# Performance work log

Hardware: AMD Instinct MI355X
Metric: run time of the kernel (lower is better)

The kernel has to match this reference:

```python
import jax, jax.numpy as jnp
import numpy as np

DIM = 192
HEADS = 6
HEAD_DIM = DIM // HEADS
WS = 8            # window size
N = WS * WS       # tokens per window
IN_CC = 16        # top-k kept keys per query
B, H, W = 8, 64, 64
NEG = -100.0      # value used by the torch code for masked logits
EPS_NORM = 1e-12  # F.normalize eps
EPS_LN = 1e-5     # nn.LayerNorm eps


def _rel_pos_index(ws):
    coords = np.stack(np.meshgrid(np.arange(ws), np.arange(ws), indexing='ij'))  # (2,ws,ws)
    cf = coords.reshape(2, -1)
    rel = (cf[:, :, None] - cf[:, None, :]).transpose(1, 2, 0).astype(np.int64)  # (N,N,2)
    rel[:, :, 0] += ws - 1
    rel[:, :, 1] += ws - 1
    rel[:, :, 0] *= 2 * ws - 1
    return jnp.asarray(rel.sum(-1))  # (N,N) indices into (2ws-1)^2 table

REL_IDX = _rel_pos_index(WS)


def _layer_norm(x, g, b):
    mu = jnp.mean(x, -1, keepdims=True)
    var = jnp.mean(jnp.square(x - mu), -1, keepdims=True)
    return (x - mu) * jax.lax.rsqrt(var + EPS_LN) * g + b


def _l2n(x):
    n = jnp.sqrt(jnp.sum(jnp.square(x), -1, keepdims=True))
    return x / jnp.maximum(n, EPS_NORM)


def setup_inputs() -> dict:
    key = jax.random.key(0)
    ks = jax.random.split(key, 8)
    s = 0.02
    return {
        'x': jax.random.normal(ks[0], (B, DIM, H, W), jnp.float32),
        'norm1_g': jnp.ones((DIM,), jnp.float32),
        'norm1_b': jnp.zeros((DIM,), jnp.float32),
        'qkv_w': jax.random.normal(ks[1], (3 * DIM, DIM), jnp.float32) * s,
        'qkv_b': jnp.zeros((3 * DIM,), jnp.float32),
        'proj_w': jax.random.normal(ks[2], (DIM, DIM), jnp.float32) * s,
        'proj_b': jnp.zeros((DIM,), jnp.float32),
        'rpb_table': jax.random.normal(ks[3], ((2 * WS - 1) ** 2, HEADS), jnp.float32) * s,
        'temperature': jnp.ones((HEADS, 1, 1), jnp.float32),
        'norm2_g': jnp.ones((DIM,), jnp.float32),
        'norm2_b': jnp.zeros((DIM,), jnp.float32),
        'fc1_w': jax.random.normal(ks[4], (4 * DIM, DIM), jnp.float32) * s,
        'fc1_b': jnp.zeros((4 * DIM,), jnp.float32),
        'fc2_w': jax.random.normal(ks[5], (DIM, 4 * DIM), jnp.float32) * s,
        'fc2_b': jnp.zeros((DIM,), jnp.float32),
    }


def reference(x, norm1_g, norm1_b, qkv_w, qkv_b, proj_w, proj_b, rpb_table,
              temperature, norm2_g, norm2_b, fc1_w, fc1_b, fc2_w, fc2_b):
    b, c, h, w = x.shape
    # (B,C,H,W) -> (B,L,C), pre-norm (note: the torch code norms the shortcut too)
    xs = jnp.transpose(x.reshape(b, c, h * w), (0, 2, 1))
    shortcut = _layer_norm(xs, norm1_g, norm1_b)  # (B,L,C)

    # window partition: (B,H,W,C) -> (B*nWh*nWw, N, C); shift_size=0, no padding (H,W % WS == 0)
    xin = shortcut.reshape(b, h // WS, WS, w // WS, WS, c)
    xin = jnp.transpose(xin, (0, 1, 3, 2, 4, 5)).reshape(-1, N, c)
    B_ = xin.shape[0]

    qkv = (xin @ qkv_w.T + qkv_b).reshape(B_, N, 3, HEADS, HEAD_DIM)
    qkv = jnp.transpose(qkv, (2, 0, 3, 1, 4))  # (3, B_, h, N, d)
    q, k, v = qkv[0], qkv[1], qkv[2]

    # cosine attention with learned per-head temperature
    attn = jnp.einsum('bhnd,bhmd->bhnm', _l2n(q), _l2n(k)) * temperature  # (B_,h,N,N)

    # top-k sparsification: keep IN_CC largest logits per query (threshold == kth value;
    # equivalent to the torch topk+scatter mask for distinct values)
    kth = jax.lax.top_k(attn, IN_CC)[0][..., -1:]
    attn = jnp.where(attn >= kth, attn, NEG)

    # relative position bias gather: (N,N,h) -> (h,N,N)
    rpb = jnp.transpose(rpb_table[REL_IDX], (2, 0, 1))
    attn = jax.nn.softmax(attn + rpb[None], axis=-1)

    out = jnp.einsum('bhnm,bhmd->bhnd', attn, v)
    out = jnp.transpose(out, (0, 2, 1, 3)).reshape(B_, N, c)
    out = out @ proj_w.T + proj_b

    # window reverse -> (B, L, C)
    out = out.reshape(b, h // WS, w // WS, WS, WS, c)
    out = jnp.transpose(out, (0, 1, 3, 2, 4, 5)).reshape(b, h * w, c)

    x2 = shortcut + out  # drop_path = identity (eval)
    hdn = _layer_norm(x2, norm2_g, norm2_b)
    hdn = jax.nn.gelu(hdn @ fc1_w.T + fc1_b, approximate=False) @ fc2_w.T + fc2_b
    x2 = x2 + hdn

    # back to (B,C,H,W)
    return jnp.transpose(x2, (0, 2, 1)).reshape(b, c, h, w)
```

## Files before the change

### kernel.cpp

```cpp
#include <hip/hip_runtime.h>
#include <hip/hip_bf16.h>
#include <math.h>

#define DIM     192
#define HEADS   6
#define HEAD_DIM 32
#define NTOK    64
#define IN_CC   16
#define TTOT    32768
#define NWIN    512

using bf16x8 = __attribute__((ext_vector_type(8))) short;
using f32x4  = __attribute__((ext_vector_type(4))) float;
typedef unsigned short ushort_t;

__device__ __forceinline__ ushort_t f2bt(float f) {
    unsigned u = __float_as_uint(f);
    u += 0x7fffu + ((u >> 16) & 1u);
    return (ushort_t)(u >> 16);
}
__device__ __forceinline__ unsigned pk2t(float a, float b) {
    return (unsigned)f2bt(a) | ((unsigned)f2bt(b) << 16);
}
__device__ __forceinline__ ushort_t f2b(float f) {
    __bf16 h = (__bf16)f;
    ushort_t u;
    __builtin_memcpy(&u, &h, 2);
    return u;
}
__device__ __forceinline__ unsigned pk2(float a, float b) {
    return (unsigned)f2b(a) | ((unsigned)f2b(b) << 16);
}
__device__ __forceinline__ float b2f(ushort_t u) {
    return __uint_as_float(((unsigned)u) << 16);
}
__device__ __forceinline__ float m3(float a, float b, float c) {
    return fmaxf(fmaxf(a, b), c);
}

__global__ __launch_bounds__(256) void prep_kernel(
    const float* __restrict__ s0, const float* __restrict__ s1,
    const float* __restrict__ s2, const float* __restrict__ s3,
    ushort_t* __restrict__ d0, ushort_t* __restrict__ d1,
    ushort_t* __restrict__ d2, ushort_t* __restrict__ d3,
    const float* __restrict__ x, const float* __restrict__ g,
    const float* __restrict__ bb, ushort_t* __restrict__ outh)
{
    __shared__ float xs[64][193];
    __shared__ float mu_s[64], rs_s[64];
    __shared__ float gs[192], bs[192];
    const int bid = blockIdx.x;
    const int tid = threadIdx.x;

    if (bid < 432) {
        const float* src; ushort_t* dst; int off, K; bool perm = false;
        if (bid < 108)      { src = s0; dst = d0; off = bid;       K = 192; perm = true; }
        else if (bid < 144) { src = s1; dst = d1; off = bid - 108; K = 192; }
        else if (bid < 288) { src = s2; dst = d2; off = bid - 144; K = 192; }
        else                { src = s3; dst = d3; off = bid - 288; K = 768; }
        const int K8 = K >> 3;
        const int d  = (off * 256 + tid) * 4;
        const int frag = d >> 7, win = d & 127;
        const int m16w = win >> 3, k7 = win & 7;
        const int oblk = frag / K8, kblk = frag - oblk * K8;
        const int o = oblk * 16 + m16w, k = kblk * 8 + k7;
        int so = o;
        if (perm && o < 384) {
            const int s = o & 31;
            const int c = (((s >> 2) & 3) << 3) | (((s >> 4) & 1) << 2) | (s & 3);
            so = (o & ~31) | c;
        }
        float4 v = *(const float4*)(src + (size_t)so * K + k);
        ushort4 ov;
        ov.x = f2b(v.x); ov.y = f2b(v.y); ov.z = f2b(v.z); ov.w = f2b(v.w);
        *(ushort4*)(dst + d) = ov;
        return;
    }

    const int t0  = (bid - 432) * 64;
    const int b   = t0 >> 12;
    const int hw0 = t0 & 4095;
    if (tid < 192) { gs[tid] = g[tid]; bs[tid] = bb[tid]; }
    const int tok = tid & 63, qq = tid >> 6;
    const float* xb = x + (size_t)b * (DIM * 4096) + hw0 + tok;
    #pragma unroll
    for (int it = 0; it < 48; ++it) {
        int c = it * 4 + qq;
        xs[tok][c] = xb[(size_t)c * 4096];
    }
    __syncthreads();
    const int tok2 = tid >> 2, p = tid & 3;
    float sum = 0.f;
    #pragma unroll
    for (int c = 0; c < 48; ++c) sum += xs[tok2][p * 48 + c];
    sum += __shfl_xor(sum, 1);
    sum += __shfl_xor(sum, 2);
    const float m = sum * (1.0f / 192.0f);
    float ss = 0.f;
    #pragma unroll
    for (int c = 0; c < 48; ++c) { float d = xs[tok2][p * 48 + c] - m; ss += d * d; }
    ss += __shfl_xor(ss, 1);
    ss += __shfl_xor(ss, 2);
    if (p == 0) {
        mu_s[tok2] = m;
        rs_s[tok2] = 1.0f / sqrtf(ss * (1.0f / 192.0f) + 1e-5f);
    }
    __syncthreads();
    ushort_t* obh = outh + (size_t)t0 * DIM;
    #pragma unroll
    for (int it = 0; it < 48; ++it) {
        int idx = it * 256 + tid;
        int tk = idx / 192, c = idx % 192;
        obh[idx] = f2b((xs[tk][c] - mu_s[tk]) * rs_s[tk] * gs[c] + bs[c]);
    }
}

__global__ __launch_bounds__(768, 3) void attn_fused(
    const ushort_t* __restrict__ sc_h, const ushort_t* __restrict__ wqf,
    const float* __restrict__ qkv_b, const float* __restrict__ rpb_table,
    const float* __restrict__ temp, const ushort_t* __restrict__ wpf,
    const float* __restrict__ proj_b, float* __restrict__ x2)
{
    __shared__ __align__(16) char smem[127680];
    const int tid  = threadIdx.x;
    const int wave = tid >> 6, n = tid & 63;

    char* Rb = smem + wave * 4608;
    float*    Ssq = (float*)Rb;
    ushort_t* Ph  = (ushort_t*)Rb;
    char* Ab = smem + 55296 + wave * 5120;
    ushort_t* Vt  = (ushort_t*)Ab;
    float*    ksb = (float*)(Ab + 4608);
    float*    qnb = (float*)(Ab + 4864);
    float*    rpb = (float*)(smem + 116736) + wave * 228;

    const int wloc = (wave >= 6) ? 1 : 0;
    const int h    = wave - 6 * wloc;
    ushort_t* tile = (ushort_t*)(smem + wloc * 25600);
    ushort_t (*AoT)[200] = (ushort_t(*)[200])(smem + wloc * 25600);
    float* Cwi = (float*)(smem + 55296 + wave * 2304);

    const int win = blockIdx.x * 2 + wloc;
    const int b   = win >> 6;
    const int wh  = (win >> 3) & 7, ww = win & 7;
    const int wb  = b * 4096 + wh * 512 + ww * 8;
    const int i1  = n >> 3, j1 = n & 7;
    const int m16 = n & 15, quad = n >> 4;

    for (int r = n; r < 225; r += 64) rpb[r] = rpb_table[r * 6 + h];

    #pragma unroll
    for (int l = 0; l < 4; ++l) {
        const int g = h * 256 + l * 64 + n;
        const int t = (g * 2731) >> 16;
        const int r = g - t * 24;
        const int tt = wb + ((t >> 3) << 6) + (t & 7);
        uint4 v = *(const uint4*)(sc_h + (size_t)tt * 192 + r * 8);
        *(uint4*)(tile + t * 200 + r * 8) = v;
    }
    __syncthreads();

    const ushort_t* tb = tile + m16 * 200 + quad * 8;
    f32x4 pq[4][2], pk[4][2];
    #pragma unroll
    for (int i = 0; i < 4; ++i)
        #pragma unroll
        for (int j = 0; j < 2; ++j) { pq[i][j] = (f32x4)(0.0f); pk[i][j] = (f32x4)(0.0f); }
    {
        const ushort_t* WbQ = wqf + (size_t)(2 * h) * 3072 + m16 * 8;
        const ushort_t* WbK = wqf + (size_t)(12 + 2 * h) * 3072 + m16 * 8;
        for (int ks = 0; ks < 192; ks += 32) {
            bf16x8 af[4], wq2[2], wk2[2];
            #pragma unroll
            for (int i = 0; i < 4; ++i)
                af[i] = *(const bf16x8*)(tb + i * 3200 + ks);
            #pragma unroll
            for (int j = 0; j < 2; ++j) {
                wq2[j] = *(const bf16x8*)(WbQ + (size_t)(j * 24 + (ks >> 3) + quad) * 128);
                wk2[j] = *(const bf16x8*)(WbK + (size_t)(j * 24 + (ks >> 3) + quad) * 128);
            }
            #pragma unroll
            for (int i = 0; i < 4; ++i)
                #pragma unroll
                for (int j = 0; j < 2; ++j) {
                    pq[i][j] = __builtin_amdgcn_mfma_f32_16x16x32_bf16(wq2[j], af[i], pq[i][j], 0, 0, 0);
                    pk[i][j] = __builtin_amdgcn_mfma_f32_16x16x32_bf16(wk2[j], af[i], pk[i][j], 0, 0, 0);
                }
        }
    }
    bf16x8 qA[4], kB[4];
    #pragma unroll
    for (int part = 0; part < 2; ++part) {
        const int o0 = part * 192 + h * 32;
        const float4 bv0 = *(const float4*)&qkv_b[o0 + 8 * quad];
        const float4 bv1 = *(const float4*)&qkv_b[o0 + 8 * quad + 4];
        float ssq[4];
        #pragma unroll
        for (int i = 0; i < 4; ++i) {
            f32x4 v0 = part ? pk[i][0] : pq[i][0];
            f32x4 v1 = part ? pk[i][1] : pq[i][1];
            v0[0] += bv0.x; v0[1] += bv0.y; v0[2] += bv0.z; v0[3] += bv0.w;
            v1[0] += bv1.x; v1[1] += bv1.y; v1[2] += bv1.z; v1[3] += bv1.w;
            float sq = 0.f;
            #pragma unroll
            for (int r = 0; r < 4; ++r) sq += v0[r] * v0[r] + v1[r] * v1[r];
            ssq[i] = sq;
            bf16x8 fr;
            fr[0] = (short)f2bt(v0[0]); fr[1] = (short)f2bt(v0[1]);
            fr[2] = (short)f2bt(v0[2]); fr[3] = (short)f2bt(v0[3]);
            fr[4] = (short)f2bt(v1[0]); fr[5] = (short)f2bt(v1[1]);
            fr[6] = (short)f2bt(v1[2]); fr[7] = (short)f2bt(v1[3]);
            if (part == 0) qA[i] = fr; else kB[i] = fr;
        }
        #pragma unroll
        for (int i = 0; i < 4; ++i) {
            ssq[i] += __shfl_xor(ssq[i], 16);
            ssq[i] += __shfl_xor(ssq[i], 32);
        }
        if (quad == 0) {
            #pragma unroll
            for (int i = 0; i < 4; ++i) {
                if (part == 0) qnb[16 * i + m16] = ssq[i];
                else           ksb[4 * m16 + i]  = 1.0f / fmaxf(sqrtf(ssq[i]), 1e-12f);
            }
        }
    }

    f32x4 acc[4][4];
    #pragma unroll
    for (int i = 0; i < 4; ++i)
        #pragma unroll
        for (int j = 0; j < 4; ++j)
            acc[i][j] = __builtin_amdgcn_mfma_f32_16x16x32_bf16(qA[i], kB[j], (f32x4)(0.0f), 0, 0, 0);

    {
        f32x4 pv[4][2];
        #pragma unroll
        for (int i = 0; i < 4; ++i)
            #pragma unroll
            for (int j = 0; j < 2; ++j) pv[i][j] = (f32x4)(0.0f);
        const ushort_t* WbV = wqf + (size_t)(24 + 2 * h) * 3072 + m16 * 8;
        for (int ks = 0; ks < 192; ks += 32) {
            bf16x8 af[4], wv2[2];
            #pragma unroll
            for (int i = 0; i < 4; ++i)
                af[i] = *(const bf16x8*)(tb + i * 3200 + ks);
            #pragma unroll
            for (int j = 0; j < 2; ++j)
                wv2[j] = *(const bf16x8*)(WbV + (size_t)(j * 24 + (ks >> 3) + quad) * 128);
            #pragma unroll
            for (int i = 0; i < 4; ++i)
                #pragma unroll
                for (int j = 0; j < 2; ++j)
                    pv[i][j] = __builtin_amdgcn_mfma_f32_16x16x32_bf16(wv2[j], af[i], pv[i][j], 0, 0, 0);
        }
        const int o0 = 384 + h * 32;
        const float4 bv0 = *(const float4*)&qkv_b[o0 + quad * 4];
        const float4 bv1 = *(const float4*)&qkv_b[o0 + 16 + quad * 4];
        #pragma unroll
        for (int i = 0; i < 4; ++i) {
            f32x4 v0 = pv[i][0], v1 = pv[i][1];
            v0[0] += bv0.x; v0[1] += bv0.y; v0[2] += bv0.z; v0[3] += bv0.w;
            v1[0] += bv1.x; v1[1] += bv1.y; v1[2] += bv1.z; v1[3] += bv1.w;
            #pragma unroll
            for (int r = 0; r < 4; ++r) {
                Vt[(quad * 4 + r) * 72 + 4 * m16 + i]      = f2bt(v0[r]);
                Vt[(16 + quad * 4 + r) * 72 + 4 * m16 + i] = f2bt(v1[r]);
            }
        }
    }

    __syncthreads();

    float s[64];
    #pragma unroll
    for (int i = 0; i < 4; ++i) {
        #pragma unroll
        for (int r = 0; r < 4; ++r) {
            f32x4 vv = { acc[i][0][r], acc[i][1][r], acc[i][2][r], acc[i][3][r] };
            *(f32x4*)&Ssq[(4 * quad + r) * 68 + 4 * m16] = vv;
        }
        if ((n >> 4) == i) {
            #pragma unroll
            for (int c = 0; c < 16; ++c)
                *(float4*)&s[4 * c] = *(const float4*)&Ssq[(n & 15) * 68 + 4 * c];
        }
    }

    const float qs = temp[h] / fmaxf(sqrtf(qnb[n]), 1e-12f);
    #pragma unroll
    for (int c = 0; c < 16; ++c) {
        float4 kv = *(const float4*)&ksb[4 * c];
        s[4*c+0] *= qs * kv.x; s[4*c+1] *= qs * kv.y;
        s[4*c+2] *= qs * kv.z; s[4*c+3] *= qs * kv.w;
    }

    float thr = 1e30f;
    for (int it = 0; it < IN_CC; ++it) {
        #define MK(c) ((s[(c)] < thr) ? s[(c)] : -1e30f)
        float w[22];
        #pragma unroll
        for (int g = 0; g < 21; ++g) w[g] = m3(MK(3*g), MK(3*g+1), MK(3*g+2));
        w[21] = MK(63);
        #undef MK
        float y[8];
        #pragma unroll
        for (int g = 0; g < 7; ++g) y[g] = m3(w[3*g], w[3*g+1], w[3*g+2]);
        y[7] = w[21];
        thr = m3(m3(y[0], y[1], y[2]), m3(y[3], y[4], y[5]), fmaxf(y[6], y[7]));
    }

    const int basen = i1 * 15 + j1;
    float mxp[8];
    #pragma unroll
    for (int c = 0; c < 64; ++c) {
        const int m = 16 * (c & 3) + (c >> 2);
        const int i2 = m >> 3, j2 = m & 7;
        float vv = ((s[c] >= thr) ? s[c] : -100.0f)
                 + rpb[basen + (7 - i2) * 15 + (7 - j2)];
        s[c] = vv;
        if (c < 8) mxp[c] = vv; else mxp[c & 7] = fmaxf(mxp[c & 7], vv);
    }
    const float mx = m3(m3(mxp[0], mxp[1], mxp[2]), m3(mxp[3], mxp[4], mxp[5]),
                        fmaxf(mxp[6], mxp[7]));
    float sum = 0.f;
    #pragma unroll
    for (int c = 0; c < 64; ++c) { float e = __expf(s[c] - mx); s[c] = e; sum += e; }
    const float inv = 1.0f / sum;
    #pragma unroll
    for (int c = 0; c < 64; ++c) s[c] *= inv;

    bf16x8 vb[2][2];
    #pragma unroll
    for (int kh2 = 0; kh2 < 2; ++kh2)
        #pragma unroll
        for (int j2 = 0; j2 < 2; ++j2)
            vb[kh2][j2] = *(const bf16x8*)&Vt[(16 * j2 + m16) * 72 + kh2 * 32 + quad * 8];

    f32x4 o[4][2];
    #pragma unroll
    for (int i = 0; i < 4; ++i)
        #pragma unroll
        for (int j2 = 0; j2 < 2; ++j2)
            o[i][j2] = (f32x4)(0.0f);
    #pragma unroll
    for (int hf = 0; hf < 2; ++hf) {
        if ((n >> 5) == hf) {
            #pragma unroll
            for (int g = 0; g < 8; ++g) {
                uint4 w;
                w.x = pk2t(s[8*g+0], s[8*g+1]); w.y = pk2t(s[8*g+2], s[8*g+3]);
                w.z = pk2t(s[8*g+4], s[8*g+5]); w.w = pk2t(s[8*g+6], s[8*g+7]);
                *(uint4*)&Ph[(n & 31) * 72 + 8 * g] = w;
            }
        }
        #pragma unroll
        for (int ih = 0; ih < 2; ++ih) {
            const int i = 2 * hf + ih;
            #pragma unroll
            for (int kh2 = 0; kh2 < 2; ++kh2) {
                bf16x8 pafr = *(const bf16x8*)&Ph[(16 * ih + m16) * 72 + kh2 * 32 + quad * 8];
                o[i][0] = __builtin_amdgcn_mfma_f32_16x16x32_bf16(pafr, vb[kh2][0], o[i][0], 0, 0, 0);
                o[i][1] = __builtin_amdgcn_mfma_f32_16x16x32_bf16(pafr, vb[kh2][1], o[i][1], 0, 0, 0);
            }
        }
    }
    __syncthreads();

    #pragma unroll
    for (int i = 0; i < 4; ++i) {
        #pragma unroll
        for (int r = 0; r < 4; ++r) {
            const int row = 16 * i + 4 * quad + r;
            AoT[row][h * 32 + m16]      = f2bt(o[i][0][r]);
            AoT[row][h * 32 + 16 + m16] = f2bt(o[i][1][r]);
        }
    }
    __syncthreads();

    const int r8 = n >> 3, c4 = (n & 7) * 4;
    uint2 rv[4][2];
    #pragma unroll
    for (int i = 0; i < 4; ++i)
        #pragma unroll
        for (int q = 0; q < 2; ++q) {
            const int tok = 16 * i + 8 * q + r8;
            const int tt = wb + ((tok >> 3) << 6) + (tok & 7);
            rv[i][q] = *(const uint2*)(sc_h + (size_t)tt * 192 + h * 32 + c4);
        }

    f32x4 pacc[4][2];
    #pragma unroll
    for (int i = 0; i < 4; ++i)
        #pragma unroll
        for (int j = 0; j < 2; ++j)
            pacc[i][j] = (f32x4)(0.0f);
    const ushort_t* Wb = wpf + (size_t)(h * 2) * 24 * 128 + m16 * 8;
    for (int ks = 0; ks < 192; ks += 32) {
        bf16x8 af[4], wv[2];
        #pragma unroll
        for (int i = 0; i < 4; ++i)
            af[i] = *(const bf16x8*)&AoT[16 * i + m16][quad * 8 + ks];
        #pragma unroll
        for (int j = 0; j < 2; ++j)
            wv[j] = *(const bf16x8*)(Wb + (size_t)(j * 24 + (ks >> 3) + quad) * 128);
        #pragma unroll
        for (int i = 0; i < 4; ++i)
            #pragma unroll
            for (int j = 0; j < 2; ++j)
                pacc[i][j] = __builtin_amdgcn_mfma_f32_16x16x32_bf16(wv[j], af[i], pacc[i][j], 0, 0, 0);
    }

    const float4 bj0 = *(const float4*)&proj_b[h * 32 + quad * 4];
    const float4 bj1 = *(const float4*)&proj_b[h * 32 + 16 + quad * 4];
    #pragma unroll
    for (int i = 0; i < 4; ++i) {
        f32x4 v0 = pacc[i][0], v1 = pacc[i][1];
        v0[0] += bj0.x; v0[1] += bj0.y; v0[2] += bj0.z; v0[3] += bj0.w;
        v1[0] += bj1.x; v1[1] += bj1.y; v1[2] += bj1.z; v1[3] += bj1.w;
        *(f32x4*)&Cwi[m16 * 36 + quad * 4]      = v0;
        *(f32x4*)&Cwi[m16 * 36 + 16 + quad * 4] = v1;
        #pragma unroll
        for (int q = 0; q < 2; ++q) {
            const int row = 8 * q + r8;
            const int tok = 16 * i + row;
            const int tt = wb + ((tok >> 3) << 6) + (tok & 7);
            float4 vv = *(const float4*)&Cwi[row * 36 + c4];
            const uint2 rr = rv[i][q];
            vv.x += b2f((ushort_t)(rr.x & 0xffffu));
            vv.y += b2f((ushort_t)(rr.x >> 16));
            vv.z += b2f((ushort_t)(rr.y & 0xffffu));
            vv.w += b2f((ushort_t)(rr.y >> 16));
            *(float4*)&x2[(size_t)tt * DIM + h * 32 + c4] = vv;
        }
    }
}

__global__ __launch_bounds__(768, 3) void mlp_fused(
    const float* __restrict__ x2, const ushort_t* __restrict__ w1f,
    const ushort_t* __restrict__ w2f, const float* __restrict__ fc1_b,
    const float* __restrict__ fc2_b, const float* __restrict__ g2,
    const float* __restrict__ b2, float* __restrict__ outp)
{
    __shared__ __align__(16) char smem[103936];
    ushort_t (*h_h)[200] = (ushort_t(*)[200])smem;
    ushort_t (*a1c)[200] = (ushort_t(*)[200])(smem + 51200);
    float* gs = (float*)(smem + 102400);
    float* bs = gs + 192;

    const int tid  = threadIdx.x;
    const int wave = tid >> 6, lane = tid & 63;
    const int m16 = lane & 15, quad = lane >> 4;
    const int half = wave / 6, ow = wave - 6 * half;
    const int t0  = blockIdx.x * 128;
    const int b   = t0 >> 12;
    const int hw0 = t0 & 4095;

    if (tid < 192) { gs[tid] = g2[tid]; bs[tid] = b2[tid]; }
    __syncthreads();
    if (tid < 512) {
        const int tok = tid >> 2, p = tid & 3;
        const float* rp = x2 + (size_t)(t0 + tok) * DIM + p * 48;
        float xv[48];
        #pragma unroll
        for (int c4 = 0; c4 < 12; ++c4)
            *(float4*)&xv[c4 * 4] = *(const float4*)(rp + c4 * 4);
        float sum = 0.f;
        #pragma unroll
        for (int c = 0; c < 48; ++c) sum += xv[c];
        sum += __shfl_xor(sum, 1);
        sum += __shfl_xor(sum, 2);
        const float m = sum * (1.0f / 192.0f);
        float ss = 0.f;
        #pragma unroll
        for (int c = 0; c < 48; ++c) { float d = xv[c] - m; ss += d * d; }
        ss += __shfl_xor(ss, 1);
        ss += __shfl_xor(ss, 2);
        const float rs = 1.0f / sqrtf(ss * (1.0f / 192.0f) + 1e-5f);
        ushort_t* hp = &h_h[tok][p * 48];
        #pragma unroll
        for (int c2 = 0; c2 < 24; ++c2) {
            float v0 = (xv[2*c2]   - m) * rs * gs[p * 48 + 2*c2]   + bs[p * 48 + 2*c2];
            float v1 = (xv[2*c2+1] - m) * rs * gs[p * 48 + 2*c2+1] + bs[p * 48 + 2*c2+1];
            *(unsigned*)(hp + 2 * c2) = pk2(v0, v1);
        }
    }
    __syncthreads();

    f32x4 acc2[4][2];
    #pragma unroll
    for (int i = 0; i < 4; ++i)
        #pragma unroll
        for (int j = 0; j < 2; ++j)
            acc2[i][j] = (f32x4)(0.0f);

    for (int c = 0; c < 4; ++c) {
        f32x4 acc1[4][2];
        #pragma unroll
        for (int i = 0; i < 4; ++i)
            #pragma unroll
            for (int j = 0; j < 2; ++j)
                acc1[i][j] = (f32x4)(0.0f);
        const ushort_t* Wb1 = w1f + (size_t)(c * 12 + ow * 2) * 3072 + m16 * 8;
        for (int ks = 0; ks < 192; ks += 32) {
            bf16x8 af[4], wv[2];
            #pragma unroll
            for (int i = 0; i < 4; ++i)
                af[i] = *(const bf16x8*)&h_h[half * 64 + 16 * i + m16][quad * 8 + ks];
            #pragma unroll
            for (int j = 0; j < 2; ++j)
                wv[j] = *(const bf16x8*)(Wb1 + (size_t)(j * 24 + (ks >> 3) + quad) * 128);
            #pragma unroll
            for (int i = 0; i < 4; ++i)
                #pragma unroll
                for (int j = 0; j < 2; ++j)
                    acc1[i][j] = __builtin_amdgcn_mfma_f32_16x16x32_bf16(wv[j], af[i], acc1[i][j], 0, 0, 0);
        }
        #pragma unroll
        for (int j = 0; j < 2; ++j) {
            const int o = c * 192 + ow * 32 + 16 * j + quad * 4;
            const float4 bv = *(const float4*)&fc1_b[o];
            #pragma unroll
            for (int i = 0; i < 4; ++i) {
                f32x4 v = acc1[i][j];
                v[0] += bv.x; v[1] += bv.y; v[2] += bv.z; v[3] += bv.w;
                #pragma unroll
                for (int r = 0; r < 4; ++r) {
                    float xg = v[r];
                    float e1 = __expf(xg * (1.5957691f + 0.0713548f * xg * xg)) + 1.0f;
                    v[r] = xg - xg * __builtin_amdgcn_rcpf(e1);
                }
                uint2 pkd;
                pkd.x = pk2(v[0], v[1]); pkd.y = pk2(v[2], v[3]);
                *(uint2*)&a1c[half * 64 + 16 * i + m16][ow * 32 + 16 * j + quad * 4] = pkd;
            }
        }
        __syncthreads();
        const ushort_t* Wb2 = w2f + (size_t)(ow * 2) * 12288 + m16 * 8;
        for (int ks = 0; ks < 192; ks += 32) {
            bf16x8 af2[4], wv2[2];
            #pragma unroll
            for (int i = 0; i < 4; ++i)
                af2[i] = *(const bf16x8*)&a1c[half * 64 + 16 * i + m16][quad * 8 + ks];
            #pragma unroll
            for (int j = 0; j < 2; ++j)
                wv2[j] = *(const bf16x8*)(Wb2 + (size_t)(j * 96 + c * 24 + (ks >> 3) + quad) * 128);
            #pragma unroll
            for (int i = 0; i < 4; ++i)
                #pragma unroll
                for (int j = 0; j < 2; ++j)
                    acc2[i][j] = __builtin_amdgcn_mfma_f32_16x16x32_bf16(wv2[j], af2[i], acc2[i][j], 0, 0, 0);
        }
        __syncthreads();
    }

    float* Cw = (float*)(smem + wave * 4608);
    float4 b2j[2];
    #pragma unroll
    for (int j = 0; j < 2; ++j)
        b2j[j] = *(const float4*)&fc2_b[ow * 32 + 16 * j + quad * 4];
    #pragma unroll
    for (int p = 0; p < 2; ++p) {
        #pragma unroll
        for (int ih = 0; ih < 2; ++ih) {
            const int i = 2 * p + ih;
            #pragma unroll
            for (int j = 0; j < 2; ++j) {
                f32x4 v = acc2[i][j];
                v[0] += b2j[j].x; v[1] += b2j[j].y; v[2] += b2j[j].z; v[3] += b2j[j].w;
                *(f32x4*)&Cw[(ih * 16 + m16) * 36 + 16 * j + quad * 4] = v;
            }
        }
        #pragma unroll
        for (int q = 0; q < 4; ++q) {
            const int idx = q * 64 + lane;
            const int cc = idx >> 3, t4 = (idx & 7) * 4;
            const int o  = ow * 32 + cc;
            const int tb = t0 + half * 64 + p * 32 + t4;
            float4 vv;
            vv.x = Cw[(t4 + 0) * 36 + cc] + x2[(size_t)(tb + 0) * DIM + o];
            vv.y = Cw[(t4 + 1) * 36 + cc] + x2[(size_t)(tb + 1) * DIM + o];
            vv.z = Cw[(t4 + 2) * 36 + cc] + x2[(size_t)(tb + 2) * DIM + o];
            vv.w = Cw[(t4 + 3) * 36 + cc] + x2[(size_t)(tb + 3) * DIM + o];
            *(float4*)&outp[(size_t)b * (DIM * 4096) + (size_t)o * 4096
                            + hw0 + half * 64 + p * 32 + t4] = vv;
        }
    }
}

extern "C" void kernel_launch(void* const* d_in, const int* in_sizes, int n_in,
                              void* d_out, int out_size, void* d_ws, size_t ws_size,
                              hipStream_t stream)
{
    const float* x        = (const float*)d_in[0];
    const float* norm1_g  = (const float*)d_in[1];
    const float* norm1_b  = (const float*)d_in[2];
    const float* qkv_w    = (const float*)d_in[3];
    const float* qkv_b    = (const float*)d_in[4];
    const float* proj_w   = (const float*)d_in[5];
    const float* proj_b   = (const float*)d_in[6];
    const float* rpbt     = (const float*)d_in[7];
    const float* temp     = (const float*)d_in[8];
    const float* norm2_g  = (const float*)d_in[9];
    const float* norm2_b  = (const float*)d_in[10];
    const float* fc1_w    = (const float*)d_in[11];
    const float* fc1_b    = (const float*)d_in[12];
    const float* fc2_w    = (const float*)d_in[13];
    const float* fc2_b    = (const float*)d_in[14];
    float* out = (float*)d_out;

    char* wsb = (char*)d_ws;
    ushort_t* shortcut_h = (ushort_t*)wsb;
    float*    x2         = (float*)(wsb + 12582912);
    ushort_t* wq  = (ushort_t*)(wsb + 125829120);
    ushort_t* wp  = wq + 110592;
    ushort_t* w1  = wp + 36864;
    ushort_t* w2  = w1 + 147456;

    hipLaunchKernelGGL(prep_kernel, dim3(432 + TTOT / 64), dim3(256), 0, stream,
                       qkv_w, proj_w, fc1_w, fc2_w, wq, wp, w1, w2,
                       x, norm1_g, norm1_b, shortcut_h);
    hipLaunchKernelGGL(attn_fused, dim3(NWIN / 2), dim3(768), 0, stream,
                       shortcut_h, wq, qkv_b, rpbt, temp, wp, proj_b, x2);
    hipLaunchKernelGGL(mlp_fused, dim3(TTOT / 128), dim3(768), 0, stream,
                       x2, w1, w2, fc1_b, fc2_b, norm2_g, norm2_b, out);
}
```

Before: 188.3 us.

## Fuse attention and MLP kernels, keep x2 residual in shared memory

Merges the attention+projection kernel with the LayerNorm2+MLP kernel so the intermediate x2 (fp32, 25 MB) stays in LDS instead of being written to and re-read from global memory. Each block now processes its two windows through the MLP in two passes of 64 tokens, with 12 waves split across token halves and output column groups. This removes one launch and global round trip, but raises LDS to about 157 KB per block, which likely limits occupancy to one block per CU. The MLP now does smaller per-wave tiles, and the final output stores are strided scalar writes into the window layout.

```diff
diff --git a/kernel.cpp b/kernel.cpp
--- a/kernel.cpp
+++ b/kernel.cpp
@@ -37,6 +37,7 @@
 __device__ __forceinline__ float m3(float a, float b, float c) {
     return fmaxf(fmaxf(a, b), c);
 }
+#define F4C(v, r) ((r) == 0 ? (v).x : (r) == 1 ? (v).y : (r) == 2 ? (v).z : (v).w)
 
 __global__ __launch_bounds__(256) void prep_kernel(
     const float* __restrict__ s0, const float* __restrict__ s1,
@@ -115,13 +116,16 @@
     }
 }
 
-__global__ __launch_bounds__(768, 3) void attn_fused(
+__global__ __launch_bounds__(768, 3) void attn_mlp_fused(
     const ushort_t* __restrict__ sc_h, const ushort_t* __restrict__ wqf,
     const float* __restrict__ qkv_b, const float* __restrict__ rpb_table,
     const float* __restrict__ temp, const ushort_t* __restrict__ wpf,
-    const float* __restrict__ proj_b, float* __restrict__ x2)
+    const float* __restrict__ proj_b, const ushort_t* __restrict__ w1f,
+    const ushort_t* __restrict__ w2f, const float* __restrict__ fc1_b,
+    const float* __restrict__ fc2_b, const float* __restrict__ g2,
+    const float* __restrict__ b2, float* __restrict__ outp)
 {
-    __shared__ __align__(16) char smem[127680];
+    __shared__ __align__(16) char smem[157184];
     const int tid  = threadIdx.x;
     const int wave = tid >> 6, n = tid & 63;
 
@@ -138,7 +142,11 @@
     const int h    = wave - 6 * wloc;
     ushort_t* tile = (ushort_t*)(smem + wloc * 25600);
     ushort_t (*AoT)[200] = (ushort_t(*)[200])(smem + wloc * 25600);
-    float* Cwi = (float*)(smem + 55296 + wave * 2304);
+    float* x2L = (float*)(smem + 55296);
+    ushort_t (*h_h)[200] = (ushort_t(*)[200])smem;
+    ushort_t (*a1c)[200] = (ushort_t(*)[200])(smem + 25600);
+    float* gs = (float*)(smem + 155648);
+    float* bs = gs + 192;
 
     const int win = blockIdx.x * 2 + wloc;
     const int b   = win >> 6;
@@ -147,6 +155,7 @@
     const int i1  = n >> 3, j1 = n & 7;
     const int m16 = n & 15, quad = n >> 4;
 
+    if (tid < 192) { gs[tid] = g2[tid]; bs[tid] = b2[tid]; }
     for (int r = n; r < 225; r += 64) rpb[r] = rpb_table[r * 6 + h];
 
     #pragma unroll
@@ -378,16 +387,15 @@
     }
     __syncthreads();
 
-    const int r8 = n >> 3, c4 = (n & 7) * 4;
-    uint2 rv[4][2];
-    #pragma unroll
-    for (int i = 0; i < 4; ++i)
-        #pragma unroll
-        for (int q = 0; q < 2; ++q) {
-            const int tok = 16 * i + 8 * q + r8;
-            const int tt = wb + ((tok >> 3) << 6) + (tok & 7);
-            rv[i][q] = *(const uint2*)(sc_h + (size_t)tt * 192 + h * 32 + c4);
-        }
+    uint2 rvv[4][2];
+    #pragma unroll
+    for (int i = 0; i < 4; ++i) {
+        const int wtok = 16 * i + m16;
+        const int tt = wb + ((wtok >> 3) << 6) + (wtok & 7);
+        #pragma unroll
+        for (int j = 0; j < 2; ++j)
+            rvv[i][j] = *(const uint2*)&sc_h[(size_t)tt * 192 + h * 32 + 16 * j + quad * 4];
+    }
 
     f32x4 pacc[4][2];
     #pragma unroll
@@ -418,172 +426,135 @@
         f32x4 v0 = pacc[i][0], v1 = pacc[i][1];
         v0[0] += bj0.x; v0[1] += bj0.y; v0[2] += bj0.z; v0[3] += bj0.w;
         v1[0] += bj1.x; v1[1] += bj1.y; v1[2] += bj1.z; v1[3] += bj1.w;
-        *(f32x4*)&Cwi[m16 * 36 + quad * 4]      = v0;
-        *(f32x4*)&Cwi[m16 * 36 + 16 + quad * 4] = v1;
-        #pragma unroll
-        for (int q = 0; q < 2; ++q) {
-            const int row = 8 * q + r8;
-            const int tok = 16 * i + row;
-            const int tt = wb + ((tok >> 3) << 6) + (tok & 7);
-            float4 vv = *(const float4*)&Cwi[row * 36 + c4];
-            const uint2 rr = rv[i][q];
-            vv.x += b2f((ushort_t)(rr.x & 0xffffu));
-            vv.y += b2f((ushort_t)(rr.x >> 16));
-            vv.z += b2f((ushort_t)(rr.y & 0xffffu));
-            vv.w += b2f((ushort_t)(rr.y >> 16));
-            *(float4*)&x2[(size_t)tt * DIM + h * 32 + c4] = vv;
-        }
-    }
-}
-
-__global__ __launch_bounds__(768, 3) void mlp_fused(
-    const float* __restrict__ x2, const ushort_t* __restrict__ w1f,
-    const ushort_t* __restrict__ w2f, const float* __restrict__ fc1_b,
-    const float* __restrict__ fc2_b, const float* __restrict__ g2,
-    const float* __restrict__ b2, float* __restrict__ outp)
-{
-    __shared__ __align__(16) char smem[103936];
-    ushort_t (*h_h)[200] = (ushort_t(*)[200])smem;
-    ushort_t (*a1c)[200] = (ushort_t(*)[200])(smem + 51200);
-    float* gs = (float*)(smem + 102400);
-    float* bs = gs + 192;
-
-    const int tid  = threadIdx.x;
-    const int wave = tid >> 6, lane = tid & 63;
-    const int m16 = lane & 15, quad = lane >> 4;
-    const int half = wave / 6, ow = wave - 6 * half;
-    const int t0  = blockIdx.x * 128;
-    const int b   = t0 >> 12;
-    const int hw0 = t0 & 4095;
-
-    if (tid < 192) { gs[tid] = g2[tid]; bs[tid] = b2[tid]; }
-    __syncthreads();
-    if (tid < 512) {
-        const int tok = tid >> 2, p = tid & 3;
-        const float* rp = x2 + (size_t)(t0 + tok) * DIM + p * 48;
-        float xv[48];
-        #pragma unroll
-        for (int c4 = 0; c4 < 12; ++c4)
-            *(float4*)&xv[c4 * 4] = *(const float4*)(rp + c4 * 4);
-        float sum = 0.f;
-        #pragma unroll
-        for (int c = 0; c < 48; ++c) sum += xv[c];
-        sum += __shfl_xor(sum, 1);
-        sum += __shfl_xor(sum, 2);
-        const float m = sum * (1.0f / 192.0f);
-        float ss = 0.f;
-        #pragma unroll
-        for (int c = 0; c < 48; ++c) { float d = xv[c] - m; ss += d * d; }
-        ss += __shfl_xor(ss, 1);
-        ss += __shfl_xor(ss, 2);
-        const float rs = 1.0f / sqrtf(ss * (1.0f / 192.0f) + 1e-5f);
-        ushort_t* hp = &h_h[tok][p * 48];
-        #pragma unroll
-        for (int c2 = 0; c2 < 24; ++c2) {
-            float v0 = (xv[2*c2]   - m) * rs * gs[p * 48 + 2*c2]   + bs[p * 48 + 2*c2];
-            float v1 = (xv[2*c2+1] - m) * rs * gs[p * 48 + 2*c2+1] + bs[p * 48 + 2*c2+1];
-            *(unsigned*)(hp + 2 * c2) = pk2(v0, v1);
-        }
-    }
-    __syncthreads();
-
-    f32x4 acc2[4][2];
-    #pragma unroll
-    for (int i = 0; i < 4; ++i)
-        #pragma unroll
-        for (int j = 0; j < 2; ++j)
-            acc2[i][j] = (f32x4)(0.0f);
-
-    for (int c = 0; c < 4; ++c) {
-        f32x4 acc1[4][2];
-        #pragma unroll
-        for (int i = 0; i < 4; ++i)
+        const uint2 r0 = rvv[i][0], r1 = rvv[i][1];
+        v0[0] += b2f((ushort_t)(r0.x & 0xffffu)); v0[1] += b2f((ushort_t)(r0.x >> 16));
+        v0[2] += b2f((ushort_t)(r0.y & 0xffffu)); v0[3] += b2f((ushort_t)(r0.y >> 16));
+        v1[0] += b2f((ushort_t)(r1.x & 0xffffu)); v1[1] += b2f((ushort_t)(r1.x >> 16));
+        v1[2] += b2f((ushort_t)(r1.y & 0xffffu)); v1[3] += b2f((ushort_t)(r1.y >> 16));
+        float* xr = &x2L[(size_t)(wloc * 64 + 16 * i + m16) * 196 + h * 32 + quad * 4];
+        *(f32x4*)xr        = v0;
+        *(f32x4*)(xr + 16) = v1;
+    }
+    __syncthreads();
+
+    const int th = wloc, ow = h;
+    for (int p = 0; p < 2; ++p) {
+        if (tid < 512) {
+            const int tok = tid >> 3, pp = tid & 7;
+            const float* xr = &x2L[(size_t)(p * 64 + tok) * 196 + pp * 24];
+            float xv[24];
+            #pragma unroll
+            for (int c6 = 0; c6 < 6; ++c6)
+                *(float4*)&xv[c6 * 4] = *(const float4*)(xr + c6 * 4);
+            float sum2 = 0.f;
+            #pragma unroll
+            for (int c = 0; c < 24; ++c) sum2 += xv[c];
+            sum2 += __shfl_xor(sum2, 1);
+            sum2 += __shfl_xor(sum2, 2);
+            sum2 += __shfl_xor(sum2, 4);
+            const float mm = sum2 * (1.0f / 192.0f);
+            float ss2 = 0.f;
+            #pragma unroll
+            for (int c = 0; c < 24; ++c) { float d = xv[c] - mm; ss2 += d * d; }
+            ss2 += __shfl_xor(ss2, 1);
+            ss2 += __shfl_xor(ss2, 2);
+            ss2 += __shfl_xor(ss2, 4);
+            const float rs = 1.0f / sqrtf(ss2 * (1.0f / 192.0f) + 1e-5f);
+            ushort_t* hp = &h_h[tok][pp * 24];
+            #pragma unroll
+            for (int c2 = 0; c2 < 12; ++c2) {
+                float v0 = (xv[2*c2]   - mm) * rs * gs[pp * 24 + 2*c2]   + bs[pp * 24 + 2*c2];
+                float v1 = (xv[2*c2+1] - mm) * rs * gs[pp * 24 + 2*c2+1] + bs[pp * 24 + 2*c2+1];
+                *(unsigned*)(hp + 2 * c2) = pk2(v0, v1);
+            }
+        }
+        __syncthreads();
+
+        f32x4 acc2[2][2];
+        #pragma unroll
+        for (int i = 0; i < 2; ++i)
             #pragma unroll
             for (int j = 0; j < 2; ++j)
-                acc1[i][j] = (f32x4)(0.0f);
-        const ushort_t* Wb1 = w1f + (size_t)(c * 12 + ow * 2) * 3072 + m16 * 8;
-        for (int ks = 0; ks < 192; ks += 32) {
-            bf16x8 af[4], wv[2];
-            #pragma unroll
-            for (int i = 0; i < 4; ++i)
-                af[i] = *(const bf16x8*)&h_h[half * 64 + 16 * i + m16][quad * 8 + ks];
-            #pragma unroll
-            for (int j = 0; j < 2; ++j)
-                wv[j] = *(const bf16x8*)(Wb1 + (size_t)(j * 24 + (ks >> 3) + quad) * 128);
-            #pragma unroll
-            for (int i = 0; i < 4; ++i)
+                acc2[i][j] = (f32x4)(0.0f);
+
+        for (int c = 0; c < 4; ++c) {
+            f32x4 acc1[2][2];
+            #pragma unroll
+            for (int i = 0; i < 2; ++i)
                 #pragma unroll
                 for (int j = 0; j < 2; ++j)
-                    acc1[i][j] = __builtin_amdgcn_mfma_f32_16x16x32_bf16(wv[j], af[i], acc1[i][j], 0, 0, 0);
-        }
+                    acc1[i][j] = (f32x4)(0.0f);
+            const ushort_t* Wb1 = w1f + (size_t)(c * 12 + ow * 2) * 3072 + m16 * 8;
+            for (int ks = 0; ks < 192; ks += 32) {
+                bf16x8 af[2], wv[2];
+                #pragma unroll
+                for (int i = 0; i < 2; ++i)
+                    af[i] = *(const bf16x8*)&h_h[th * 32 + 16 * i + m16][quad * 8 + ks];
+                #pragma unroll
+                for (int j = 0; j < 2; ++j)
+                    wv[j] = *(const bf16x8*)(Wb1 + (size_t)(j * 24 + (ks >> 3) + quad) * 128);
+                #pragma unroll
+                for (int i = 0; i < 2; ++i)
+                    #pragma unroll
+                    for (int j = 0; j < 2; ++j)
+                        acc1[i][j] = __builtin_amdgcn_mfma_f32_16x16x32_bf16(wv[j], af[i], acc1[i][j], 0, 0, 0);
+            }
+            #pragma unroll
+            for (int j = 0; j < 2; ++j) {
+                const int oo = c * 192 + ow * 32 + 16 * j + quad * 4;
+                const float4 bv = *(const float4*)&fc1_b[oo];
+                #pragma unroll
+                for (int i = 0; i < 2; ++i) {
+                    f32x4 v = acc1[i][j];
+                    v[0] += bv.x; v[1] += bv.y; v[2] += bv.z; v[3] += bv.w;
+                    #pragma unroll
+                    for (int r = 0; r < 4; ++r) {
+                        float xg = v[r];
+                        float e1 = __expf(xg * (1.5957691f + 0.0713548f * xg * xg)) + 1.0f;
+                        v[r] = xg - xg * __builtin_amdgcn_rcpf(e1);
+                    }
+                    uint2 pkd;
+                    pkd.x = pk2(v[0], v[1]); pkd.y = pk2(v[2], v[3]);
+                    *(uint2*)&a1c[th * 32 + 16 * i + m16][ow * 32 + 16 * j + quad * 4] = pkd;
+                }
+            }
+            __syncthreads();
+            const ushort_t* Wb2 = w2f + (size_t)(ow * 2) * 12288 + m16 * 8;
+            for (int ks = 0; ks < 192; ks += 32) {
+                bf16x8 af2[2], wv2[2];
+                #pragma unroll
+                for (int i = 0; i < 2; ++i)
+                    af2[i] = *(const bf16x8*)&a1c[th * 32 + 16 * i + m16][quad * 8 + ks];
+                #pragma unroll
+                for (int j = 0; j < 2; ++j)
+                    wv2[j] = *(const bf16x8*)(Wb2 + (size_t)(j * 96 + c * 24 + (ks >> 3) + quad) * 128);
+                #pragma unroll
+                for (int i = 0; i < 2; ++i)
+                    #pragma unroll
+                    for (int j = 0; j < 2; ++j)
+                        acc2[i][j] = __builtin_amdgcn_mfma_f32_16x16x32_bf16(wv2[j], af2[i], acc2[i][j], 0, 0, 0);
+            }
+            __syncthreads();
+        }
+
+        const int winp = blockIdx.x * 2 + p;
+        const int bb2 = winp >> 6, whp = (winp >> 3) & 7, wwp = winp & 7;
+        float* outb = outp + (size_t)bb2 * (DIM * 4096);
         #pragma unroll
         for (int j = 0; j < 2; ++j) {
-            const int o = c * 192 + ow * 32 + 16 * j + quad * 4;
-            const float4 bv = *(const float4*)&fc1_b[o];
-            #pragma unroll
-            for (int i = 0; i < 4; ++i) {
-                f32x4 v = acc1[i][j];
-                v[0] += bv.x; v[1] += bv.y; v[2] += bv.z; v[3] += bv.w;
+            const float4 b2v = *(const float4*)&fc2_b[ow * 32 + 16 * j + quad * 4];
+            #pragma unroll
+            for (int i = 0; i < 2; ++i) {
+                const int wtok = th * 32 + 16 * i + m16;
+                const int hw = (whp * 8 + (wtok >> 3)) * 64 + wwp * 8 + (wtok & 7);
+                const float* xrr = &x2L[(size_t)(p * 64 + wtok) * 196];
                 #pragma unroll
                 for (int r = 0; r < 4; ++r) {
-                    float xg = v[r];
-                    float e1 = __expf(xg * (1.5957691f + 0.0713548f * xg * xg)) + 1.0f;
-                    v[r] = xg - xg * __builtin_amdgcn_rcpf(e1);
+                    const int oo = ow * 32 + 16 * j + quad * 4 + r;
+                    outb[(size_t)oo * 4096 + hw] =
+                        acc2[i][j][r] + F4C(b2v, r) + xrr[oo];
                 }
-                uint2 pkd;
-                pkd.x = pk2(v[0], v[1]); pkd.y = pk2(v[2], v[3]);
-                *(uint2*)&a1c[half * 64 + 16 * i + m16][ow * 32 + 16 * j + quad * 4] = pkd;
-            }
-        }
-        __syncthreads();
-        const ushort_t* Wb2 = w2f + (size_t)(ow * 2) * 12288 + m16 * 8;
-        for (int ks = 0; ks < 192; ks += 32) {
-            bf16x8 af2[4], wv2[2];
-            #pragma unroll
-            for (int i = 0; i < 4; ++i)
-                af2[i] = *(const bf16x8*)&a1c[half * 64 + 16 * i + m16][quad * 8 + ks];
-            #pragma unroll
-            for (int j = 0; j < 2; ++j)
-                wv2[j] = *(const bf16x8*)(Wb2 + (size_t)(j * 96 + c * 24 + (ks >> 3) + quad) * 128);
-            #pragma unroll
-            for (int i = 0; i < 4; ++i)
-                #pragma unroll
-                for (int j = 0; j < 2; ++j)
-                    acc2[i][j] = __builtin_amdgcn_mfma_f32_16x16x32_bf16(wv2[j], af2[i], acc2[i][j], 0, 0, 0);
-        }
-        __syncthreads();
-    }
-
-    float* Cw = (float*)(smem + wave * 4608);
-    float4 b2j[2];
-    #pragma unroll
-    for (int j = 0; j < 2; ++j)
-        b2j[j] = *(const float4*)&fc2_b[ow * 32 + 16 * j + quad * 4];
-    #pragma unroll
-    for (int p = 0; p < 2; ++p) {
-        #pragma unroll
-        for (int ih = 0; ih < 2; ++ih) {
-            const int i = 2 * p + ih;
-            #pragma unroll
-            for (int j = 0; j < 2; ++j) {
-                f32x4 v = acc2[i][j];
-                v[0] += b2j[j].x; v[1] += b2j[j].y; v[2] += b2j[j].z; v[3] += b2j[j].w;
-                *(f32x4*)&Cw[(ih * 16 + m16) * 36 + 16 * j + quad * 4] = v;
-            }
-        }
-        #pragma unroll
-        for (int q = 0; q < 4; ++q) {
-            const int idx = q * 64 + lane;
-            const int cc = idx >> 3, t4 = (idx & 7) * 4;
-            const int o  = ow * 32 + cc;
-            const int tb = t0 + half * 64 + p * 32 + t4;
-            float4 vv;
-            vv.x = Cw[(t4 + 0) * 36 + cc] + x2[(size_t)(tb + 0) * DIM + o];
-            vv.y = Cw[(t4 + 1) * 36 + cc] + x2[(size_t)(tb + 1) * DIM + o];
-            vv.z = Cw[(t4 + 2) * 36 + cc] + x2[(size_t)(tb + 2) * DIM + o];
-            vv.w = Cw[(t4 + 3) * 36 + cc] + x2[(size_t)(tb + 3) * DIM + o];
-            *(float4*)&outp[(size_t)b * (DIM * 4096) + (size_t)o * 4096
-                            + hw0 + half * 64 + p * 32 + t4] = vv;
+            }
         }
     }
 }
@@ -611,7 +582,6 @@
 
     char* wsb = (char*)d_ws;
     ushort_t* shortcut_h = (ushort_t*)wsb;
-    float*    x2         = (float*)(wsb + 12582912);
     ushort_t* wq  = (ushort_t*)(wsb + 125829120);
     ushort_t* wp  = wq + 110592;
     ushort_t* w1  = wp + 36864;
@@ -620,8 +590,7 @@
     hipLaunchKernelGGL(prep_kernel, dim3(432 + TTOT / 64), dim3(256), 0, stream,
                        qkv_w, proj_w, fc1_w, fc2_w, wq, wp, w1, w2,
                        x, norm1_g, norm1_b, shortcut_h);
-    hipLaunchKernelGGL(attn_fused, dim3(NWIN / 2), dim3(768), 0, stream,
-                       shortcut_h, wq, qkv_b, rpbt, temp, wp, proj_b, x2);
-    hipLaunchKernelGGL(mlp_fused, dim3(TTOT / 128), dim3(768), 0, stream,
-                       x2, w1, w2, fc1_b, fc2_b, norm2_g, norm2_b, out);
-}
+    hipLaunchKernelGGL(attn_mlp_fused, dim3(NWIN / 2), dim3(768), 0, stream,
+                       shortcut_h, wq, qkv_b, rpbt, temp, wp, proj_b,
+                       w1, w2, fc1_b, fc2_b, norm2_g, norm2_b, out);
+}
```

New measurement: 190.5 us. About the same (+1.2%).
